# Performance work log

Measured on AMD Instinct MI355X. Metric: run time of the kernel, lower is better.

The kernel has to match this reference:

```python
import jax, jax.numpy as jnp
import numpy as np

BETA = 0.25


def setup_inputs() -> dict:
    key = jax.random.key(0)
    k1, k2 = jax.random.split(key)
    z = jax.random.normal(k1, (16, 2048, 64), dtype=jnp.float32)
    emb = jax.random.uniform(k2, (8192, 64), dtype=jnp.float32)  # uniform_() init
    return {"z": z, "emb": emb}


def reference(z, emb):
    # z: [B, N, D], emb: [K, D]; use_norm=False so norm is identity.
    B, N, D = z.shape
    zf = z.reshape(-1, D)                                   # [B*N, D]
    # Squared euclidean distances; argmin is identical to cdist(p=2) argmin.
    d2 = (
        jnp.sum(zf * zf, axis=1, keepdims=True)
        - 2.0 * (zf @ emb.T)
        + jnp.sum(emb * emb, axis=1)
    )                                                       # [B*N, K]
    idx = jnp.argmin(d2, axis=1)                            # [B*N]
    z_q = emb[idx].reshape(z.shape)                         # [B, N, D]
    loss = BETA * jnp.mean((jax.lax.stop_gradient(z_q) - z) ** 2) + jnp.mean(
        (z_q - jax.lax.stop_gradient(z)) ** 2
    )
    z_q_st = z + jax.lax.stop_gradient(z_q - z)             # straight-through
    return z_q_st, idx, loss
```

## Files before the change

### kernel.cpp

```cpp
#include <hip/hip_runtime.h>
#include <hip/hip_bf16.h>
#include <math.h>

#define D 64
#define K_CODES 8192
#define M_QUERIES 32768
#define SLICES 8
#define CODES_PER_SLICE (K_CODES / SLICES)
#define CHUNK 32
#define NCHUNK (CODES_PER_SLICE / CHUNK)
#define QPB 128
#define TAU_V 4e-3f

typedef __attribute__((ext_vector_type(8))) short bf16x8;
typedef __attribute__((ext_vector_type(4))) float f32x4;
typedef __attribute__((ext_vector_type(16))) float f32x16;

__device__ __forceinline__ unsigned short f2bf(float x) {
    __hip_bfloat16 h = __float2bfloat16(x);
    return *reinterpret_cast<unsigned short*>(&h);
}
__device__ __forceinline__ float bf2f(unsigned short s) {
    __hip_bfloat16 h;
    *reinterpret_cast<unsigned short*>(&h) = s;
    return __bfloat162float(h);
}
__device__ __forceinline__ void gld_lds16(const void* g, void* l) {
    __builtin_amdgcn_global_load_lds(
        (const __attribute__((address_space(1))) void*)g,
        (__attribute__((address_space(3))) void*)l, 16, 0, 0);
}
__device__ __forceinline__ void gld_lds4(const void* g, void* l) {
    __builtin_amdgcn_global_load_lds(
        (const __attribute__((address_space(1))) void*)g,
        (__attribute__((address_space(3))) void*)l, 4, 0, 0);
}

__global__ __launch_bounds__(256) void k0_split(const float* __restrict__ emb,
                                                unsigned short* __restrict__ e_hi,
                                                unsigned short* __restrict__ e_lo,
                                                float* __restrict__ halfee,
                                                double* __restrict__ eed,
                                                int* __restrict__ ws_cnt) {
    const int t = threadIdx.x;
    const int grp = blockIdx.x;
    if (grp == 0 && t == 0) *ws_cnt = 0;
    const int u = t & 7;
#pragma unroll
    for (int it = 0; it < 2; ++it) {
        const int r = (t >> 3) + it * 32;
        const int code = grp * 64 + r;
        const float* src = emb + ((size_t)code * 64 + u * 8);
        float4 f0 = *(const float4*)(src);
        float4 f1 = *(const float4*)(src + 4);
        float f[8] = {f0.x, f0.y, f0.z, f0.w, f1.x, f1.y, f1.z, f1.w};
        bf16x8 h, lo;
        float s = 0.f;
        double sd = 0.0;
#pragma unroll
        for (int j = 0; j < 8; ++j) {
            float e = f[j];
            s += e * e;
            sd += (double)e * (double)e;
            unsigned short hh = f2bf(e);
            h[j]  = (short)hh;
            lo[j] = (short)f2bf(e - bf2f(hh));
        }
        const int c32 = code >> 5, r32 = code & 31;
        size_t off = (size_t)c32 * 4096 + (size_t)(u * 32 + r32) * 16;
        *(bf16x8*)((char*)e_hi + off) = h;
        *(bf16x8*)((char*)e_lo + off) = lo;
        s += __shfl_xor(s, 1);
        s += __shfl_xor(s, 2);
        s += __shfl_xor(s, 4);
        sd += __shfl_xor(sd, 1);
        sd += __shfl_xor(sd, 2);
        sd += __shfl_xor(sd, 4);
        if (u == 0) {
            halfee[code] = 0.5f * s + 128.0f;
            eed[code]    = sd;
        }
    }
}

__global__ __launch_bounds__(256, 1) void k1_mfma(const float* __restrict__ z,
                                                  const unsigned short* __restrict__ e_hi,
                                                  const unsigned short* __restrict__ e_lo,
                                                  const float* __restrict__ halfee,
                                                  float4* __restrict__ ws_part) {
    __shared__ __align__(16) unsigned short ldshi[2][CHUNK * 64];
    __shared__ __align__(16) unsigned short ldslo[2][CHUNK * 64];
    __shared__ __align__(16) float ldshe[2][CHUNK];

    const int tid = threadIdx.x;
    const int wid = tid >> 6;
    const int l   = tid & 63;
    const int col = l & 31;
    const int hi  = l >> 5;
    const int slice = blockIdx.y;
    const int chunk0 = slice * NCHUNK;
    const int cbase0 = slice * CODES_PER_SLICE;

    const int qw0 = blockIdx.x * QPB + wid * 32;
    const int qrow = qw0 + col;
    bf16x8 qh[4], ql[4];
#pragma unroll
    for (int kk = 0; kk < 4; ++kk) {
        const float* src = z + (size_t)qrow * D + kk * 16 + hi * 8;
        float4 f0 = *(const float4*)(src);
        float4 f1 = *(const float4*)(src + 4);
        float f[8] = {f0.x, f0.y, f0.z, f0.w, f1.x, f1.y, f1.z, f1.w};
        bf16x8 h, lo;
#pragma unroll
        for (int j = 0; j < 8; ++j) {
            float x = -f[j];
            unsigned short hh = f2bf(x);
            float r = x - bf2f(hh);
            h[j]  = (short)hh;
            lo[j] = (short)f2bf(r);
        }
        qh[kk] = h;
        ql[kk] = lo;
    }

    float g1 = 1e30f, g2 = 1e30f;
    int   gi = 0x7fffffff;

#define STAGE(buf, c1)                                                           \
    {                                                                            \
        size_t cb = (size_t)(chunk0 + (c1)) * 4096 + wid * 1024 + l * 16;        \
        gld_lds16((const char*)e_hi + cb, (char*)&ldshi[buf][0] + wid * 1024);   \
        gld_lds16((const char*)e_lo + cb, (char*)&ldslo[buf][0] + wid * 1024);   \
        if (tid < 32)                                                            \
            gld_lds4((const char*)halfee + (size_t)(chunk0 + (c1)) * 128 + tid * 4, \
                     (char*)&ldshe[buf][0]);                                     \
    }

#define MFMA_CHUNK(bufc, acc)                                                    \
    {                                                                            \
        const char*  bh  = (const char*)ldshi[bufc];                             \
        const char*  bl  = (const char*)ldslo[bufc];                             \
        const float* bhe = ldshe[bufc];                                          \
        _Pragma("unroll") for (int g4 = 0; g4 < 4; ++g4) {                       \
            f32x4 he4 = *(const f32x4*)(bhe + g4 * 8 + 4 * hi);                  \
            _Pragma("unroll") for (int j = 0; j < 4; ++j)                        \
                acc[g4 * 4 + j] = he4[j];                                        \
        }                                                                        \
        _Pragma("unroll") for (int kk = 0; kk < 4; ++kk) {                       \
            int a0 = ((kk * 2 + hi) * 32 + col) * 16;       \
            bf16x8 ah = *(const bf16x8*)(bh + a0);                               \
            bf16x8 al = *(const bf16x8*)(bl + a0);                               \
            acc = __builtin_amdgcn_mfma_f32_32x32x16_bf16(ah, qh[kk], acc, 0, 0, 0); \
            acc = __builtin_amdgcn_mfma_f32_32x32x16_bf16(ah, ql[kk], acc, 0, 0, 0); \
            acc = __builtin_amdgcn_mfma_f32_32x32x16_bf16(al, qh[kk], acc, 0, 0, 0); \
        }                                                                        \
    }

#define TOP2T(acc, cbase)                                                        \
    {                                                                            \
        float t1[8], t2[8];                                                      \
        _Pragma("unroll") for (int i = 0; i < 8; ++i) {                          \
            float va = __int_as_float((__float_as_int(acc[2 * i])     & 0xFFFFFFF0) | (2 * i));     \
            float vb = __int_as_float((__float_as_int(acc[2 * i + 1]) & 0xFFFFFFF0) | (2 * i + 1)); \
            t1[i] = fminf(va, vb);                                               \
            t2[i] = fmaxf(va, vb);                                               \
        }                                                                        \
        _Pragma("unroll") for (int s = 4; s > 0; s >>= 1) {                      \
            _Pragma("unroll") for (int i = 0; i < s; ++i) {                      \
                float m2c = fminf(t2[i], t2[i + s]);                             \
                t2[i] = __builtin_amdgcn_fmed3f(t1[i], t1[i + s], m2c);          \
                t1[i] = fminf(t1[i], t1[i + s]);                                 \
            }                                                                    \
        }                                                                        \
        float m1p = t1[0], m2p = t2[0];                                          \
        int p1 = __float_as_int(m1p) & 15;                                       \
        int code = (cbase) + (p1 & 3) + 8 * (p1 >> 2) + 4 * hi;                  \
        bool lt = m1p < g1;                                                      \
        g2 = fminf(lt ? g1 : g2, lt ? m2p : m1p);                                \
        g1 = lt ? m1p : g1;                                                      \
        gi = lt ? code : gi;                                                     \
    }

    f32x16 accE, accO;

    STAGE(0, 0);
    __syncthreads();
    STAGE(1, 1);
    MFMA_CHUNK(0, accE);
    __syncthreads();
    for (int cc = 1; cc + 1 < NCHUNK; cc += 2) {
        STAGE(0, cc + 1);
        MFMA_CHUNK(1, accO);
        TOP2T(accE, cbase0 + (cc - 1) * CHUNK);
        __syncthreads();
        if (cc + 2 < NCHUNK) STAGE(1, cc + 2);
        MFMA_CHUNK(0, accE);
        TOP2T(accO, cbase0 + cc * CHUNK);
        __syncthreads();
    }
    MFMA_CHUNK(1, accO);
    TOP2T(accE, cbase0 + (NCHUNK - 2) * CHUNK);
    TOP2T(accO, cbase0 + (NCHUNK - 1) * CHUNK);

    {
        float o1 = __shfl_xor(g1, 32);
        float o2 = __shfl_xor(g2, 32);
        int   oi = __shfl_xor(gi, 32);
        bool  take = (o1 < g1) || (o1 == g1 && oi < gi);
        float n2   = take ? fminf(o2, g1) : fminf(g2, o1);
        g1 = take ? o1 : g1;
        gi = take ? oi : gi;
        g2 = n2;
        if (l < 32) {
            int q = qw0 + col;
            ws_part[(size_t)q * SLICES + slice] =
                make_float4(g1, g2, __int_as_float(gi), 0.f);
        }
    }
#undef STAGE
#undef MFMA_CHUNK
#undef TOP2T
}

__global__ __launch_bounds__(256) void k1b_merge(const float4* __restrict__ ws_part,
                                                 int* __restrict__ ws_idx,
                                                 int* __restrict__ ws_cnt,
                                                 int* __restrict__ ws_list,
                                                 float* __restrict__ out) {
    int q = blockIdx.x * blockDim.x + threadIdx.x;
    float m1 = 1e30f, m2 = 1e30f;
    int   i1 = 0x7fffffff;
#pragma unroll
    for (int s = 0; s < SLICES; ++s) {
        float4 p = ws_part[(size_t)q * SLICES + s];
        float v1 = p.x, v2 = p.y;
        int   vi = __float_as_int(p.z);
        if (v1 < m1 || (v1 == m1 && vi < i1)) { m2 = fminf(m1, v2); m1 = v1; i1 = vi; }
        else                                  { m2 = fminf(m2, v1); }
    }
    ws_idx[q] = i1;
    out[(size_t)M_QUERIES * D + q] = (float)i1;
    if (m2 - m1 < TAU_V) {
        int r = atomicAdd(ws_cnt, 1);
        ws_list[r] = q;
    }
}

__global__ __launch_bounds__(256) void k2_rescue(const float* __restrict__ z,
                                                 const float* __restrict__ emb,
                                                 const double* __restrict__ eed,
                                                 const int* __restrict__ ws_cnt,
                                                 const int* __restrict__ ws_list,
                                                 int* __restrict__ ws_idx,
                                                 float* __restrict__ out) {
    __shared__ float  zrow[D];
    __shared__ double rv[256];
    __shared__ int    ri[256];
    const int cnt = *ws_cnt;
    for (int r = blockIdx.x; r < cnt; r += gridDim.x) {
        const int q = ws_list[r];
        __syncthreads();
        if (threadIdx.x < D) zrow[threadIdx.x] = z[(size_t)q * D + threadIdx.x];
        __syncthreads();
        double best = 1e300;
        int    bi   = 0x7fffffff;
        for (int c = threadIdx.x; c < K_CODES; c += 256) {
            const float4* er = (const float4*)(emb + (size_t)c * D);
            double dot = 0.0;
#pragma unroll
            for (int k = 0; k < 16; ++k) {
                float4 e = er[k];
                dot += (double)zrow[4 * k + 0] * (double)e.x
                     + (double)zrow[4 * k + 1] * (double)e.y
                     + (double)zrow[4 * k + 2] * (double)e.z
                     + (double)zrow[4 * k + 3] * (double)e.w;
            }
            double s = fma(-2.0, dot, eed[c]);
            if (s < best) { best = s; bi = c; }
        }
        rv[threadIdx.x] = best;
        ri[threadIdx.x] = bi;
        __syncthreads();
        for (int s = 128; s > 0; s >>= 1) {
            if (threadIdx.x < s) {
                double ov = rv[threadIdx.x + s];
                int    oi = ri[threadIdx.x + s];
                if (ov < rv[threadIdx.x] || (ov == rv[threadIdx.x] && oi < ri[threadIdx.x])) {
                    rv[threadIdx.x] = ov;
                    ri[threadIdx.x] = oi;
                }
            }
            __syncthreads();
        }
        if (threadIdx.x == 0) {
            ws_idx[q] = ri[0];
            out[(size_t)M_QUERIES * D + q] = (float)ri[0];
        }
        __syncthreads();
    }
}

__global__ __launch_bounds__(256) void k3_gather(const float* __restrict__ emb,
                                                 const float* __restrict__ z,
                                                 const int* __restrict__ ws_idx,
                                                 float* __restrict__ out,
                                                 float* __restrict__ partial) {
    __shared__ float sb[256];
    int g = blockIdx.x * 256 + threadIdx.x;
    int q = g >> 6, d = g & 63;
    int id = ws_idx[q];
    float e = emb[(size_t)id * D + d];
    out[g] = e;
    float df = e - z[g];
    sb[threadIdx.x] = df * df;
    __syncthreads();
    for (int s = 128; s > 0; s >>= 1) {
        if (threadIdx.x < s) sb[threadIdx.x] += sb[threadIdx.x + s];
        __syncthreads();
    }
    if (threadIdx.x == 0) partial[blockIdx.x] = sb[0];
}

__global__ __launch_bounds__(256) void k4_loss(const float* __restrict__ partial,
                                               float* __restrict__ out) {
    __shared__ double sb[256];
    double s = 0.0;
    for (int i = threadIdx.x; i < (M_QUERIES * D) / 256; i += 256) s += (double)partial[i];
    sb[threadIdx.x] = s;
    __syncthreads();
    for (int st = 128; st > 0; st >>= 1) {
        if (threadIdx.x < st) sb[threadIdx.x] += sb[threadIdx.x + st];
        __syncthreads();
    }
    if (threadIdx.x == 0)
        out[(size_t)M_QUERIES * D + M_QUERIES] =
            (float)(1.25 * sb[0] / (double)((size_t)M_QUERIES * D));
}

extern "C" void kernel_launch(void* const* d_in, const int* in_sizes, int n_in,
                              void* d_out, int out_size, void* d_ws, size_t ws_size,
                              hipStream_t stream) {
    const float* z   = (const float*)d_in[0];
    const float* emb = (const float*)d_in[1];
    float* out = (float*)d_out;
    char*  ws  = (char*)d_ws;

    unsigned short* e_hi    = (unsigned short*)(ws);
    unsigned short* e_lo    = (unsigned short*)(ws + 1048576);
    float*          halfee  = (float*)(ws + 2097152);
    double*         eed     = (double*)(ws + 2129920);
    float4*         ws_part = (float4*)(ws + 2195456);
    int*            ws_idx  = (int*)(ws + 2195456 + 4194304);
    int*            ws_cnt  = (int*)(ws + 2195456 + 4194304 + 131072);
    int*            ws_list = (int*)(ws + 2195456 + 4194304 + 131136);
    float*          partial = (float*)(ws + 2195456 + 4194304 + 262208);

    k0_split<<<K_CODES / 64, 256, 0, stream>>>(emb, e_hi, e_lo, halfee, eed, ws_cnt);

    dim3 g1(M_QUERIES / QPB, SLICES);
    k1_mfma<<<g1, 256, 0, stream>>>(z, e_hi, e_lo, halfee, ws_part);

    k1b_merge<<<M_QUERIES / 256, 256, 0, stream>>>(ws_part, ws_idx, ws_cnt, ws_list, out);

    k2_rescue<<<256, 256, 0, stream>>>(z, emb, eed, ws_cnt, ws_list, ws_idx, out);

    k3_gather<<<(M_QUERIES * D) / 256, 256, 0, stream>>>(emb, z, ws_idx, out, partial);

    k4_loss<<<1, 256, 0, stream>>>(partial, out);
}
```

Measured before the change: 198.3 us.

## Fuse merge, rescue and loss; derive loss from distances; vectorize gather

Computes per-query |z|^2 in the MFMA kernel and derives the commitment loss from the minimum distance, removing the separate gather-side squared-difference reduction and the final loss kernel. Merges the top-2 merge and the exact fp64 rescue into one kernel using a per-block shared-memory list instead of a global atomic list. The gather kernel becomes a pure float4 copy. This trades fewer launches and less memory traffic for float atomic loss accumulation, a slight precision change, and rescue work that is concentrated in fewer blocks.

```diff
diff --git a/kernel.cpp b/kernel.cpp
--- a/kernel.cpp
+++ b/kernel.cpp
@@ -41,10 +41,10 @@
                                                 unsigned short* __restrict__ e_lo,
                                                 float* __restrict__ halfee,
                                                 double* __restrict__ eed,
-                                                int* __restrict__ ws_cnt) {
+                                                float* __restrict__ loss_ptr) {
     const int t = threadIdx.x;
     const int grp = blockIdx.x;
-    if (grp == 0 && t == 0) *ws_cnt = 0;
+    if (grp == 0 && t == 0) *loss_ptr = 0.0f;
     const int u = t & 7;
 #pragma unroll
     for (int it = 0; it < 2; ++it) {
@@ -104,6 +104,7 @@
     const int qw0 = blockIdx.x * QPB + wid * 32;
     const int qrow = qw0 + col;
     bf16x8 qh[4], ql[4];
+    float szz = 0.f;
 #pragma unroll
     for (int kk = 0; kk < 4; ++kk) {
         const float* src = z + (size_t)qrow * D + kk * 16 + hi * 8;
@@ -113,6 +114,7 @@
         bf16x8 h, lo;
 #pragma unroll
         for (int j = 0; j < 8; ++j) {
+            szz += f[j] * f[j];
             float x = -f[j];
             unsigned short hh = f2bf(x);
             float r = x - bf2f(hh);
@@ -122,6 +124,7 @@
         qh[kk] = h;
         ql[kk] = lo;
     }
+    szz += __shfl_xor(szz, 32);
 
     float g1 = 1e30f, g2 = 1e30f;
     int   gi = 0x7fffffff;
@@ -214,7 +217,7 @@
         if (l < 32) {
             int q = qw0 + col;
             ws_part[(size_t)q * SLICES + slice] =
-                make_float4(g1, g2, __int_as_float(gi), 0.f);
+                make_float4(g1, g2, __int_as_float(gi), szz);
         }
     }
 #undef STAGE
@@ -222,49 +225,60 @@
 #undef TOP2T
 }
 
-__global__ __launch_bounds__(256) void k1b_merge(const float4* __restrict__ ws_part,
-                                                 int* __restrict__ ws_idx,
-                                                 int* __restrict__ ws_cnt,
-                                                 int* __restrict__ ws_list,
-                                                 float* __restrict__ out) {
-    int q = blockIdx.x * blockDim.x + threadIdx.x;
-    float m1 = 1e30f, m2 = 1e30f;
+__global__ __launch_bounds__(256) void k1b2(const float4* __restrict__ ws_part,
+                                            const float* __restrict__ z,
+                                            const float* __restrict__ emb,
+                                            const double* __restrict__ eed,
+                                            int* __restrict__ ws_idx,
+                                            float* __restrict__ out) {
+    __shared__ int   llist[256];
+    __shared__ int   lcnt;
+    __shared__ float sb[256];
+    __shared__ float zrow[D];
+    __shared__ double rv[256];
+    __shared__ int    ri[256];
+
+    const int tid = threadIdx.x;
+    if (tid == 0) lcnt = 0;
+    __syncthreads();
+
+    const int q = blockIdx.x * 256 + tid;
+    float m1 = 1e30f, m2 = 1e30f, zz = 0.f;
     int   i1 = 0x7fffffff;
 #pragma unroll
     for (int s = 0; s < SLICES; ++s) {
         float4 p = ws_part[(size_t)q * SLICES + s];
         float v1 = p.x, v2 = p.y;
         int   vi = __float_as_int(p.z);
+        zz = p.w;
         if (v1 < m1 || (v1 == m1 && vi < i1)) { m2 = fminf(m1, v2); m1 = v1; i1 = vi; }
         else                                  { m2 = fminf(m2, v1); }
     }
     ws_idx[q] = i1;
     out[(size_t)M_QUERIES * D + q] = (float)i1;
+    sb[tid] = zz + 2.0f * (m1 - 128.0f);
     if (m2 - m1 < TAU_V) {
-        int r = atomicAdd(ws_cnt, 1);
-        ws_list[r] = q;
-    }
-}
-
-__global__ __launch_bounds__(256) void k2_rescue(const float* __restrict__ z,
-                                                 const float* __restrict__ emb,
-                                                 const double* __restrict__ eed,
-                                                 const int* __restrict__ ws_cnt,
-                                                 const int* __restrict__ ws_list,
-                                                 int* __restrict__ ws_idx,
-                                                 float* __restrict__ out) {
-    __shared__ float  zrow[D];
-    __shared__ double rv[256];
-    __shared__ int    ri[256];
-    const int cnt = *ws_cnt;
-    for (int r = blockIdx.x; r < cnt; r += gridDim.x) {
-        const int q = ws_list[r];
-        __syncthreads();
-        if (threadIdx.x < D) zrow[threadIdx.x] = z[(size_t)q * D + threadIdx.x];
+        int r = atomicAdd(&lcnt, 1);
+        llist[r] = q;
+    }
+    __syncthreads();
+    for (int s = 128; s > 0; s >>= 1) {
+        if (tid < s) sb[tid] += sb[tid + s];
+        __syncthreads();
+    }
+    if (tid == 0)
+        atomicAdd(out + (size_t)M_QUERIES * D + M_QUERIES,
+                  sb[0] * (1.25f / (float)((size_t)M_QUERIES * D)));
+
+    const int cnt = lcnt;
+    for (int r = 0; r < cnt; ++r) {
+        const int rq = llist[r];
+        __syncthreads();
+        if (tid < D) zrow[tid] = z[(size_t)rq * D + tid];
         __syncthreads();
         double best = 1e300;
         int    bi   = 0x7fffffff;
-        for (int c = threadIdx.x; c < K_CODES; c += 256) {
+        for (int c = tid; c < K_CODES; c += 256) {
             const float4* er = (const float4*)(emb + (size_t)c * D);
             double dot = 0.0;
 #pragma unroll
@@ -278,63 +292,36 @@
             double s = fma(-2.0, dot, eed[c]);
             if (s < best) { best = s; bi = c; }
         }
-        rv[threadIdx.x] = best;
-        ri[threadIdx.x] = bi;
+        rv[tid] = best;
+        ri[tid] = bi;
         __syncthreads();
         for (int s = 128; s > 0; s >>= 1) {
-            if (threadIdx.x < s) {
-                double ov = rv[threadIdx.x + s];
-                int    oi = ri[threadIdx.x + s];
-                if (ov < rv[threadIdx.x] || (ov == rv[threadIdx.x] && oi < ri[threadIdx.x])) {
-                    rv[threadIdx.x] = ov;
-                    ri[threadIdx.x] = oi;
+            if (tid < s) {
+                double ov = rv[tid + s];
+                int    oi = ri[tid + s];
+                if (ov < rv[tid] || (ov == rv[tid] && oi < ri[tid])) {
+                    rv[tid] = ov;
+                    ri[tid] = oi;
                 }
             }
             __syncthreads();
         }
-        if (threadIdx.x == 0) {
-            ws_idx[q] = ri[0];
-            out[(size_t)M_QUERIES * D + q] = (float)ri[0];
-        }
-        __syncthreads();
+        if (tid == 0) {
+            ws_idx[rq] = ri[0];
+            out[(size_t)M_QUERIES * D + rq] = (float)ri[0];
+        }
     }
 }
 
 __global__ __launch_bounds__(256) void k3_gather(const float* __restrict__ emb,
-                                                 const float* __restrict__ z,
                                                  const int* __restrict__ ws_idx,
-                                                 float* __restrict__ out,
-                                                 float* __restrict__ partial) {
-    __shared__ float sb[256];
-    int g = blockIdx.x * 256 + threadIdx.x;
-    int q = g >> 6, d = g & 63;
+                                                 float* __restrict__ out) {
+    int g4 = blockIdx.x * 256 + threadIdx.x;
+    int q  = g4 >> 4;
+    int dd = g4 & 15;
     int id = ws_idx[q];
-    float e = emb[(size_t)id * D + d];
-    out[g] = e;
-    float df = e - z[g];
-    sb[threadIdx.x] = df * df;
-    __syncthreads();
-    for (int s = 128; s > 0; s >>= 1) {
-        if (threadIdx.x < s) sb[threadIdx.x] += sb[threadIdx.x + s];
-        __syncthreads();
-    }
-    if (threadIdx.x == 0) partial[blockIdx.x] = sb[0];
-}
-
-__global__ __launch_bounds__(256) void k4_loss(const float* __restrict__ partial,
-                                               float* __restrict__ out) {
-    __shared__ double sb[256];
-    double s = 0.0;
-    for (int i = threadIdx.x; i < (M_QUERIES * D) / 256; i += 256) s += (double)partial[i];
-    sb[threadIdx.x] = s;
-    __syncthreads();
-    for (int st = 128; st > 0; st >>= 1) {
-        if (threadIdx.x < st) sb[threadIdx.x] += sb[threadIdx.x + st];
-        __syncthreads();
-    }
-    if (threadIdx.x == 0)
-        out[(size_t)M_QUERIES * D + M_QUERIES] =
-            (float)(1.25 * sb[0] / (double)((size_t)M_QUERIES * D));
+    float4 v = ((const float4*)(emb + (size_t)id * D))[dd];
+    ((float4*)out)[g4] = v;
 }
 
 extern "C" void kernel_launch(void* const* d_in, const int* in_sizes, int n_in,
@@ -351,20 +338,15 @@
     double*         eed     = (double*)(ws + 2129920);
     float4*         ws_part = (float4*)(ws + 2195456);
     int*            ws_idx  = (int*)(ws + 2195456 + 4194304);
-    int*            ws_cnt  = (int*)(ws + 2195456 + 4194304 + 131072);
-    int*            ws_list = (int*)(ws + 2195456 + 4194304 + 131136);
-    float*          partial = (float*)(ws + 2195456 + 4194304 + 262208);
-
-    k0_split<<<K_CODES / 64, 256, 0, stream>>>(emb, e_hi, e_lo, halfee, eed, ws_cnt);
+
+    float* loss_ptr = out + (size_t)M_QUERIES * D + M_QUERIES;
+
+    k0_split<<<K_CODES / 64, 256, 0, stream>>>(emb, e_hi, e_lo, halfee, eed, loss_ptr);
 
     dim3 g1(M_QUERIES / QPB, SLICES);
     k1_mfma<<<g1, 256, 0, stream>>>(z, e_hi, e_lo, halfee, ws_part);
 
-    k1b_merge<<<M_QUERIES / 256, 256, 0, stream>>>(ws_part, ws_idx, ws_cnt, ws_list, out);
-
-    k2_rescue<<<256, 256, 0, stream>>>(z, emb, eed, ws_cnt, ws_list, ws_idx, out);
-
-    k3_gather<<<(M_QUERIES * D) / 256, 256, 0, stream>>>(emb, z, ws_idx, out, partial);
-
-    k4_loss<<<1, 256, 0, stream>>>(partial, out);
-}
+    k1b2<<<M_QUERIES / 256, 256, 0, stream>>>(ws_part, z, emb, eed, ws_idx, out);
+
+    k3_gather<<<(M_QUERIES * D / 4) / 256, 256, 0, stream>>>(emb, ws_idx, out);
+}
```

Measured after the change: 479.6 us. +141.9%, slower.
